# Kernel tuning notes

Measured on AMD Instinct MI355X. Metric: run time of the kernel, lower is better.

The kernel has to match this reference:

```python
import jax, jax.numpy as jnp
import numpy as np

B, T, E = 4, 2048, 1024
H, HS = 16, 64
FF = 4 * E
EPS = 1e-5


def _layer_norm(x, g, b):
    mu = jnp.mean(x, axis=-1, keepdims=True)
    var = jnp.mean(jnp.square(x - mu), axis=-1, keepdims=True)
    return (x - mu) * jax.lax.rsqrt(var + EPS) * g + b


def setup_inputs() -> dict:
    key = jax.random.key(0)
    ks = jax.random.split(key, 8)
    s_e = 1.0 / np.sqrt(E)
    s_hs = 1.0 / np.sqrt(H * HS)
    s_ff = 1.0 / np.sqrt(FF)
    return {
        "x": jax.random.normal(ks[0], (B, T, E), dtype=jnp.float32),
        # weights stored as [in, out] (transpose of torch's [out, in])
        "qkv_w": jax.random.uniform(ks[1], (E, 3 * H * HS), minval=-s_e, maxval=s_e),
        "attn_proj_w": jax.random.uniform(ks[2], (H * HS, E), minval=-s_hs, maxval=s_hs),
        "attn_proj_b": jax.random.uniform(ks[3], (E,), minval=-s_hs, maxval=s_hs),
        "ln1_g": jnp.ones((E,), jnp.float32),
        "ln1_b": jnp.zeros((E,), jnp.float32),
        "ln2_g": jnp.ones((E,), jnp.float32),
        "ln2_b": jnp.zeros((E,), jnp.float32),
        "ff_w1": jax.random.uniform(ks[4], (E, FF), minval=-s_e, maxval=s_e),
        "ff_b1": jax.random.uniform(ks[5], (FF,), minval=-s_e, maxval=s_e),
        "ff_w2": jax.random.uniform(ks[6], (FF, E), minval=-s_ff, maxval=s_ff),
        "ff_b2": jax.random.uniform(ks[7], (E,), minval=-s_ff, maxval=s_ff),
    }


def reference(x, qkv_w, attn_proj_w, attn_proj_b, ln1_g, ln1_b, ln2_g, ln2_b,
              ff_w1, ff_b1, ff_w2, ff_b2):
    b, t, _ = x.shape
    # --- pre-LN causal self-attention ---
    h = _layer_norm(x, ln1_g, ln1_b)
    qkv = h @ qkv_w                                  # [B,T,3*H*HS]
    q, k, v = jnp.split(qkv, 3, axis=-1)
    q = q.reshape(b, t, H, HS).transpose(0, 2, 1, 3)  # [B,H,T,HS]
    k = k.reshape(b, t, H, HS).transpose(0, 2, 1, 3)
    v = v.reshape(b, t, H, HS).transpose(0, 2, 1, 3)
    scores = jnp.einsum('bhqd,bhkd->bhqk', q, k) * (HS ** -0.5)
    causal = jnp.tril(jnp.ones((t, t), dtype=bool))
    scores = jnp.where(causal, scores, -jnp.inf)
    attn = jax.nn.softmax(scores, axis=-1)
    out = jnp.einsum('bhqk,bhkd->bhqd', attn, v)      # [B,H,T,HS]
    out = out.transpose(0, 2, 1, 3).reshape(b, t, H * HS)
    x = x + out @ attn_proj_w + attn_proj_b
    # --- pre-LN feed-forward ---
    h2 = _layer_norm(x, ln2_g, ln2_b)
    ff = jax.nn.relu(h2 @ ff_w1 + ff_b1) @ ff_w2 + ff_b2
    return x + ff
```

## Files before the change

### kernel.cpp

```cpp
#include <hip/hip_runtime.h>
#include <math.h>

#define B_ 4
#define T_ 2048
#define E_ 1024
#define H_ 16
#define HS_ 64
#define FF_ 4096
#define M_ (B_ * T_)
#define QKV3_ (3 * H_ * HS_)

typedef short bf16x8 __attribute__((ext_vector_type(8)));
typedef short bf16x4 __attribute__((ext_vector_type(4)));
typedef float f32x4 __attribute__((ext_vector_type(4)));

__device__ __forceinline__ unsigned short f2bf(float f) {
    unsigned int u = __float_as_uint(f);
    return (unsigned short)((u + 0x7fffu + ((u >> 16) & 1u)) >> 16);
}

__device__ __forceinline__ void gload16(const void* g, void* l) {
    __builtin_amdgcn_global_load_lds(
        (const __attribute__((address_space(1))) void*)g,
        (__attribute__((address_space(3))) void*)l, 16, 0, 0);
}

__global__ __launch_bounds__(256) void wT_bf16(const float* __restrict__ W,
                                               unsigned short* __restrict__ WT,
                                               int K, int N) {
    __shared__ float t[32][33];
    const int n0 = blockIdx.x * 32, k0 = blockIdx.y * 32;
    const int tid = threadIdx.x;
#pragma unroll
    for (int i = 0; i < 4; i++) {
        const int idx = i * 256 + tid;
        const int r = idx >> 5, c = idx & 31;
        t[r][c] = W[(size_t)(k0 + r) * N + n0 + c];
    }
    __syncthreads();
#pragma unroll
    for (int i = 0; i < 4; i++) {
        const int idx = i * 256 + tid;
        const int n = idx >> 5, k = idx & 31;
        WT[(size_t)(n0 + n) * K + k0 + k] = f2bf(t[k][n]);
    }
}

__global__ __launch_bounds__(256) void ln_bf16(const float* __restrict__ x,
                                               const float* __restrict__ g,
                                               const float* __restrict__ b,
                                               unsigned short* __restrict__ out) {
    const int row = blockIdx.x;
    const int tid = threadIdx.x;
    const float4 v = ((const float4*)(x + (size_t)row * E_))[tid];
    float s = v.x + v.y + v.z + v.w;
    float ss = v.x * v.x + v.y * v.y + v.z * v.z + v.w * v.w;
    for (int off = 32; off > 0; off >>= 1) {
        s += __shfl_down(s, off);
        ss += __shfl_down(ss, off);
    }
    __shared__ float rs[4], rss[4];
    const int wid = tid >> 6;
    if ((tid & 63) == 0) { rs[wid] = s; rss[wid] = ss; }
    __syncthreads();
    const float tot = rs[0] + rs[1] + rs[2] + rs[3];
    const float tot2 = rss[0] + rss[1] + rss[2] + rss[3];
    const float mean = tot * (1.0f / E_);
    const float var = tot2 * (1.0f / E_) - mean * mean;
    const float rstd = rsqrtf(var + 1e-5f);
    const float4 gv = ((const float4*)g)[tid];
    const float4 bv = ((const float4*)b)[tid];
    ushort4 o;
    o.x = f2bf((v.x - mean) * rstd * gv.x + bv.x);
    o.y = f2bf((v.y - mean) * rstd * gv.y + bv.y);
    o.z = f2bf((v.z - mean) * rstd * gv.z + bv.z);
    o.w = f2bf((v.w - mean) * rstd * gv.w + bv.w);
    ((ushort4*)(out + (size_t)row * E_))[tid] = o;
}

__device__ __forceinline__ void stage_half(const unsigned short* __restrict__ G,
                                           size_t rbase, int K, int k0,
                                           unsigned short* lds, int c) {
    const int r = c >> 3, s = c & 7;
    gload16(G + rbase + (size_t)r * K + k0 + ((s ^ (r & 7)) * 8),
            (char*)lds + c * 16);
}

template <bool BIASF, bool RELU, bool RES, bool OUTBF16>
__global__ __launch_bounds__(512) void gemm_v3(
    const unsigned short* __restrict__ A,
    const unsigned short* __restrict__ BT,
    const float* __restrict__ bias,
    const float* __restrict__ res,
    float* __restrict__ Cf,
    unsigned short* __restrict__ Cb,
    int M, int N, int K) {
    __shared__ unsigned short As[3][128 * 64];
    __shared__ unsigned short Bs[3][256 * 64];

    const int tid = threadIdx.x;
    const int lane = tid & 63;
    const int w = tid >> 6;
    const int wm = w >> 2, wn = w & 3;
    const int lm = lane & 15;
    const int kg = lane >> 4;

    const int gx = gridDim.x;
    const int nwg = gx * gridDim.y;
    const int lin = blockIdx.y * gx + blockIdx.x;
    const int cpx = nwg >> 3;
    const int swz = (lin & 7) * cpx + (lin >> 3);
    const int rowBase = (swz / gx) * 128, colBase = (swz % gx) * 256;

    const size_t rA = (size_t)rowBase * K;
    const size_t rB = (size_t)colBase * K;

    f32x4 acc[4][4];
#pragma unroll
    for (int mt = 0; mt < 4; mt++)
#pragma unroll
        for (int nt = 0; nt < 4; nt++)
#pragma unroll
            for (int r = 0; r < 4; r++) acc[mt][nt][r] = 0.0f;

    const int nk = K >> 6;
#pragma unroll
    for (int h = 0; h < 2; h++) {
        stage_half(A, rA, K, 0, As[0], h * 512 + tid);
        stage_half(BT, rB, K, 0, Bs[0], h * 1024 + tid);
        stage_half(BT, rB, K, 0, Bs[0], h * 1024 + 512 + tid);
    }
#pragma unroll
    for (int h = 0; h < 2; h++) {
        stage_half(A, rA, K, 64, As[1], h * 512 + tid);
        stage_half(BT, rB, K, 64, Bs[1], h * 1024 + tid);
        stage_half(BT, rB, K, 64, Bs[1], h * 1024 + 512 + tid);
    }
    asm volatile("s_waitcnt vmcnt(6)" ::: "memory");
    __builtin_amdgcn_s_barrier();
    __builtin_amdgcn_sched_barrier(0);

    for (int t = 0; t < nk; ++t) {
        const int cur = t % 3;
        const int nx2 = (t + 2) % 3;
        const bool doStage = (t + 2 < nk);
#pragma unroll
        for (int ks = 0; ks < 2; ++ks) {
            bf16x8 af[4], bfr[4];
#pragma unroll
            for (int mt = 0; mt < 4; mt++) {
                const int r = wm * 64 + mt * 16 + lm;
                af[mt] = *(const bf16x8*)(As[cur] + r * 64 +
                                          (((ks * 4 + kg) ^ (r & 7)) * 8));
            }
#pragma unroll
            for (int nt = 0; nt < 4; nt++) {
                const int r = wn * 64 + nt * 16 + lm;
                bfr[nt] = *(const bf16x8*)(Bs[cur] + r * 64 +
                                           (((ks * 4 + kg) ^ (r & 7)) * 8));
            }
            if (doStage) {
                stage_half(A, rA, K, (t + 2) * 64, As[nx2], ks * 512 + tid);
                stage_half(BT, rB, K, (t + 2) * 64, Bs[nx2], ks * 1024 + tid);
                stage_half(BT, rB, K, (t + 2) * 64, Bs[nx2], ks * 1024 + 512 + tid);
            }
            __builtin_amdgcn_s_barrier();
            __builtin_amdgcn_sched_barrier(0);
            __builtin_amdgcn_s_setprio(1);
#pragma unroll
            for (int mt = 0; mt < 4; mt++)
#pragma unroll
                for (int nt = 0; nt < 4; nt++)
                    acc[mt][nt] = __builtin_amdgcn_mfma_f32_16x16x32_bf16(
                        af[mt], bfr[nt], acc[mt][nt], 0, 0, 0);
            __builtin_amdgcn_s_setprio(0);
            if (ks == 0) {
                __builtin_amdgcn_s_barrier();
                __builtin_amdgcn_sched_barrier(0);
            }
        }
        if (t + 2 < nk) {
            asm volatile("s_waitcnt vmcnt(6)" ::: "memory");
        } else if (t + 1 < nk) {
            asm volatile("s_waitcnt vmcnt(0)" ::: "memory");
        }
        __builtin_amdgcn_sched_barrier(0);
        __builtin_amdgcn_s_barrier();
        __builtin_amdgcn_sched_barrier(0);
    }

#pragma unroll
    for (int mt = 0; mt < 4; mt++) {
#pragma unroll
        for (int nt = 0; nt < 4; nt++) {
            const int cg = colBase + wn * 64 + nt * 16 + lm;
#pragma unroll
            for (int r = 0; r < 4; r++) {
                const int rg = rowBase + wm * 64 + mt * 16 + kg * 4 + r;
                float v = acc[mt][nt][r];
                if (BIASF) v += bias[cg];
                if (RELU) v = fmaxf(v, 0.0f);
                if (RES) v += res[(size_t)rg * N + cg];
                if (OUTBF16) Cb[(size_t)rg * N + cg] = f2bf(v);
                else Cf[(size_t)rg * N + cg] = v;
            }
        }
    }
}

__global__ __launch_bounds__(256) void attn_mfma3(const unsigned short* __restrict__ qkv,
                                                  unsigned short* __restrict__ out) {
    __shared__ unsigned short Ks[2][64 * 64];
    __shared__ unsigned short Vt[2][64 * 72];

    const int tid = threadIdx.x;
    const int lane = tid & 63;
    const int w = tid >> 6;
    const int lm = lane & 15;
    const int kg = lane >> 4;
    const int qt = 15 - blockIdx.x;
    const int bh = blockIdx.y;
    const int b = bh >> 4, h = bh & 15;
    const int bT = b * T_;
    const int q0w = qt * 128 + w * 32;
    const float K1 = 0.18033688011f;

    bf16x8 qf[2][2];
#pragma unroll
    for (int qg = 0; qg < 2; qg++) {
        const size_t qo = (size_t)(bT + q0w + qg * 16 + lm) * QKV3_ + h * HS_;
#pragma unroll
        for (int dc = 0; dc < 2; dc++)
            qf[qg][dc] = *(const bf16x8*)(qkv + qo + dc * 32 + kg * 8);
    }

    f32x4 o[2][4];
#pragma unroll
    for (int qg = 0; qg < 2; qg++)
#pragma unroll
        for (int dt = 0; dt < 4; dt++)
#pragma unroll
            for (int r = 0; r < 4; r++) o[qg][dt][r] = 0.0f;
    float m2[2] = {-INFINITY, -INFINITY};
    float l[2] = {0.0f, 0.0f};

    const int rK = tid >> 3, chK = tid & 7;
    const int sK = (chK ^ (rK & 7)) * 8;
    const int rp = tid >> 3, chV = tid & 7;
    const int vws = (2 * rp) ^ (chV << 2);

    const size_t hK = E_ + h * HS_;
    const size_t hV = 2 * E_ + h * HS_;
    bf16x8 kA, kB, vA, vB;

#define LOADT(kvb)                                                                          \
    do {                                                                                    \
        kA = *(const bf16x8*)(qkv + (size_t)(bT + (kvb) + rK) * QKV3_ + hK + chK * 8);      \
        kB = *(const bf16x8*)(qkv + (size_t)(bT + (kvb) + rK + 32) * QKV3_ + hK + chK * 8); \
        vA = *(const bf16x8*)(qkv + (size_t)(bT + (kvb) + 2 * rp) * QKV3_ + hV + chV * 8);  \
        vB = *(const bf16x8*)(qkv + (size_t)(bT + (kvb) + 2 * rp + 1) * QKV3_ + hV + chV * 8); \
    } while (0)

    const int nt = 2 * (qt + 1);
    LOADT(0);
    for (int t = 0; t < nt; t++) {
        const int kvbase = t * 64;
        const int cb = t & 1;
        *(bf16x8*)(Ks[cb] + rK * 64 + sK) = kA;
        *(bf16x8*)(Ks[cb] + (rK + 32) * 64 + sK) = kB;
#pragma unroll
        for (int i = 0; i < 8; i++) {
            const unsigned int pv = (unsigned int)(unsigned short)vA[i] |
                                    ((unsigned int)(unsigned short)vB[i] << 16);
            *(unsigned int*)(Vt[cb] + (chV * 8 + i) * 72 + vws) = pv;
        }
        if (t + 1 < nt) LOADT((t + 1) * 64);
        asm volatile("s_waitcnt lgkmcnt(0)" ::: "memory");
        __builtin_amdgcn_s_barrier();
        __builtin_amdgcn_sched_barrier(0);
        if (kvbase > q0w + 31) continue;

        bf16x8 af[4][2];
#pragma unroll
        for (int g = 0; g < 4; g++)
#pragma unroll
            for (int dc = 0; dc < 2; dc++)
                af[g][dc] = *(const bf16x8*)(Ks[cb] + (g * 16 + lm) * 64 +
                                             (((dc * 4 + kg) ^ (lm & 7)) * 8));

        bf16x8 pa[2][2];
#pragma unroll
        for (int qg = 0; qg < 2; qg++) {
            f32x4 z = {0.0f, 0.0f, 0.0f, 0.0f};
            f32x4 s[4];
#pragma unroll
            for (int g = 0; g < 4; g++) {
                s[g] = __builtin_amdgcn_mfma_f32_16x16x32_bf16(af[g][0], qf[qg][0], z, 0, 0, 0);
                s[g] = __builtin_amdgcn_mfma_f32_16x16x32_bf16(af[g][1], qf[qg][1], s[g], 0, 0, 0);
            }
            const int qrow = q0w + qg * 16 + lm;
            float sv[16];
#pragma unroll
            for (int g = 0; g < 4; g++)
#pragma unroll
                for (int r = 0; r < 4; r++) sv[g * 4 + r] = s[g][r];
            if (kvbase + 63 > q0w + qg * 16) {
#pragma unroll
                for (int g = 0; g < 4; g++)
#pragma unroll
                    for (int r = 0; r < 4; r++) {
                        const int kv = kvbase + g * 16 + kg * 4 + r;
                        if (kv > qrow) sv[g * 4 + r] = -INFINITY;
                    }
            }
            const float mx = fmaxf(
                fmaxf(fmaxf(fmaxf(sv[0], sv[1]), fmaxf(sv[2], sv[3])),
                      fmaxf(fmaxf(sv[4], sv[5]), fmaxf(sv[6], sv[7]))),
                fmaxf(fmaxf(fmaxf(sv[8], sv[9]), fmaxf(sv[10], sv[11])),
                      fmaxf(fmaxf(sv[12], sv[13]), fmaxf(sv[14], sv[15]))));
            float mxw = fmaxf(mx, __shfl_xor(mx, 16));
            mxw = fmaxf(mxw, __shfl_xor(mxw, 32));
            const float mx2 = mxw * K1;
            if (!__all(m2[qg] > -1e30f && mx2 <= m2[qg] + 11.5f)) {
                const float m2new = fmaxf(m2[qg], mx2);
                const float alpha = exp2f(m2[qg] - m2new);
#pragma unroll
                for (int r = 0; r < 4; r++) {
                    const float ar = __shfl(alpha, kg * 4 + r);
#pragma unroll
                    for (int dt = 0; dt < 4; dt++) o[qg][dt][r] *= ar;
                }
                l[qg] *= alpha;
                m2[qg] = m2new;
            }
            float p[16];
#pragma unroll
            for (int j = 0; j < 16; j++) p[j] = exp2f(fmaf(sv[j], K1, -m2[qg]));
            float ls = (((p[0] + p[1]) + (p[2] + p[3])) + ((p[4] + p[5]) + (p[6] + p[7]))) +
                       (((p[8] + p[9]) + (p[10] + p[11])) + ((p[12] + p[13]) + (p[14] + p[15])));
            ls += __shfl_xor(ls, 16);
            ls += __shfl_xor(ls, 32);
            l[qg] += ls;
#pragma unroll
            for (int j = 0; j < 8; j++) {
                ((unsigned short*)&pa[qg][0])[j] = f2bf(p[j]);
                ((unsigned short*)&pa[qg][1])[j] = f2bf(p[8 + j]);
            }
        }

#pragma unroll
        for (int dt = 0; dt < 4; dt++) {
            const int drow = dt * 16 + lm;
            const unsigned short* vrow = Vt[cb] + drow * 72;
            const int xo = (kg * 4) ^ (((drow >> 3) & 7) << 2);
#pragma unroll
            for (int c = 0; c < 2; c++) {
                const bf16x4 lo = *(const bf16x4*)(vrow + c * 32 + xo);
                const bf16x4 hi = *(const bf16x4*)(vrow + c * 32 + (xo ^ 16));
                const bf16x8 vf = __builtin_shufflevector(lo, hi, 0, 1, 2, 3, 4, 5, 6, 7);
                o[0][dt] = __builtin_amdgcn_mfma_f32_16x16x32_bf16(pa[0][c], vf, o[0][dt], 0, 0, 0);
                o[1][dt] = __builtin_amdgcn_mfma_f32_16x16x32_bf16(pa[1][c], vf, o[1][dt], 0, 0, 0);
            }
        }
    }
#undef LOADT

#pragma unroll
    for (int qg = 0; qg < 2; qg++)
#pragma unroll
        for (int r = 0; r < 4; r++) {
            const float li = 1.0f / __shfl(l[qg], kg * 4 + r);
            const size_t ro = (size_t)(bT + q0w + qg * 16 + kg * 4 + r) * E_ + h * HS_;
#pragma unroll
            for (int dt = 0; dt < 4; dt++)
                out[ro + dt * 16 + lm] = f2bf(o[qg][dt][r] * li);
        }
}

extern "C" void kernel_launch(void* const* d_in, const int* in_sizes, int n_in,
                              void* d_out, int out_size, void* d_ws, size_t ws_size,
                              hipStream_t stream) {
    const float* x           = (const float*)d_in[0];
    const float* qkv_w       = (const float*)d_in[1];
    const float* attn_proj_w = (const float*)d_in[2];
    const float* attn_proj_b = (const float*)d_in[3];
    const float* ln1_g       = (const float*)d_in[4];
    const float* ln1_b       = (const float*)d_in[5];
    const float* ln2_g       = (const float*)d_in[6];
    const float* ln2_b       = (const float*)d_in[7];
    const float* ff_w1       = (const float*)d_in[8];
    const float* ff_b1       = (const float*)d_in[9];
    const float* ff_w2       = (const float*)d_in[10];
    const float* ff_b2       = (const float*)d_in[11];
    float* out = (float*)d_out;
    char* wsb = (char*)d_ws;

    unsigned short* wqkvT  = (unsigned short*)(wsb + 0);
    unsigned short* wprojT = (unsigned short*)(wsb + 6291456);
    unsigned short* wff1T  = (unsigned short*)(wsb + 8388608);
    unsigned short* wff2T  = (unsigned short*)(wsb + 16777216);
    unsigned short* hbuf   = (unsigned short*)(wsb + 25165824);
    unsigned short* attnb  = (unsigned short*)(wsb + 41943040);
    unsigned short* qkvb   = (unsigned short*)(wsb + 58720256);
    unsigned short* ff1b   = qkvb;

    wT_bf16<<<dim3(QKV3_ / 32, E_ / 32), 256, 0, stream>>>(qkv_w, wqkvT, E_, QKV3_);
    wT_bf16<<<dim3(E_ / 32, E_ / 32), 256, 0, stream>>>(attn_proj_w, wprojT, E_, E_);
    wT_bf16<<<dim3(FF_ / 32, E_ / 32), 256, 0, stream>>>(ff_w1, wff1T, E_, FF_);
    wT_bf16<<<dim3(E_ / 32, FF_ / 32), 256, 0, stream>>>(ff_w2, wff2T, FF_, E_);

    ln_bf16<<<M_, 256, 0, stream>>>(x, ln1_g, ln1_b, hbuf);
    gemm_v3<false, false, false, true><<<dim3(QKV3_ / 256, M_ / 128), 512, 0, stream>>>(
        hbuf, wqkvT, nullptr, nullptr, nullptr, qkvb, M_, QKV3_, E_);
    attn_mfma3<<<dim3(T_ / 128, B_ * H_), 256, 0, stream>>>(qkvb, attnb);
    gemm_v3<true, false, true, false><<<dim3(E_ / 256, M_ / 128), 512, 0, stream>>>(
        attnb, wprojT, attn_proj_b, x, out, nullptr, M_, E_, E_);
    ln_bf16<<<M_, 256, 0, stream>>>(out, ln2_g, ln2_b, hbuf);
    gemm_v3<true, true, false, true><<<dim3(FF_ / 256, M_ / 128), 512, 0, stream>>>(
        hbuf, wff1T, ff_b1, nullptr, nullptr, ff1b, M_, FF_, E_);
    gemm_v3<true, false, true, false><<<dim3(E_ / 256, M_ / 128), 512, 0, stream>>>(
        ff1b, wff2T, ff_b2, out, out, nullptr, M_, E_, FF_);
    (void)ws_size; (void)in_sizes; (void)n_in; (void)out_size;
}
```

Baseline: 570.7 us.

## Enlarge GEMM row tile to 256 with templated N tile and double buffering

Replaces the 128x256 triple-buffered GEMM with a templated kernel using 256-row tiles, a configurable N tile (256 for QKV/FF1, 128 for proj/FF2) and a two-stage LDS buffer. Loads for the next k-tile are issued at the start of each iteration and fully drained at the end. The aim is higher data reuse per block and fewer barriers per iteration. The risks are weaker latency hiding from shallower pipelining, larger register use from more accumulators, and fewer blocks for the N=1024 GEMMs.

```diff
diff --git a/kernel.cpp b/kernel.cpp
--- a/kernel.cpp
+++ b/kernel.cpp
@@ -86,8 +86,8 @@
             (char*)lds + c * 16);
 }
 
-template <bool BIASF, bool RELU, bool RES, bool OUTBF16>
-__global__ __launch_bounds__(512) void gemm_v3(
+template <int BN, int NWN, bool BIASF, bool RELU, bool RES, bool OUTBF16>
+__global__ __launch_bounds__(512, 2) void gemm_v4(
     const unsigned short* __restrict__ A,
     const unsigned short* __restrict__ BT,
     const float* __restrict__ bias,
@@ -95,13 +95,18 @@
     float* __restrict__ Cf,
     unsigned short* __restrict__ Cb,
     int M, int N, int K) {
-    __shared__ unsigned short As[3][128 * 64];
-    __shared__ unsigned short Bs[3][256 * 64];
+    constexpr int NWM = 8 / NWN;
+    constexpr int MW = 256 / NWM;
+    constexpr int M_REP = MW / 16;
+    constexpr int BPT = (BN * 64 / 8) / 512;
+
+    __shared__ unsigned short As[2][256 * 64];
+    __shared__ unsigned short Bs[2][BN * 64];
 
     const int tid = threadIdx.x;
     const int lane = tid & 63;
     const int w = tid >> 6;
-    const int wm = w >> 2, wn = w & 3;
+    const int wm = w / NWN, wn = w % NWN;
     const int lm = lane & 15;
     const int kg = lane >> 4;
 
@@ -110,14 +115,14 @@
     const int lin = blockIdx.y * gx + blockIdx.x;
     const int cpx = nwg >> 3;
     const int swz = (lin & 7) * cpx + (lin >> 3);
-    const int rowBase = (swz / gx) * 128, colBase = (swz % gx) * 256;
+    const int rowBase = (swz / gx) * 256, colBase = (swz % gx) * BN;
 
     const size_t rA = (size_t)rowBase * K;
     const size_t rB = (size_t)colBase * K;
 
-    f32x4 acc[4][4];
-#pragma unroll
-    for (int mt = 0; mt < 4; mt++)
+    f32x4 acc[M_REP][4];
+#pragma unroll
+    for (int mt = 0; mt < M_REP; mt++)
 #pragma unroll
         for (int nt = 0; nt < 4; nt++)
 #pragma unroll
@@ -125,31 +130,29 @@
 
     const int nk = K >> 6;
 #pragma unroll
-    for (int h = 0; h < 2; h++) {
-        stage_half(A, rA, K, 0, As[0], h * 512 + tid);
-        stage_half(BT, rB, K, 0, Bs[0], h * 1024 + tid);
-        stage_half(BT, rB, K, 0, Bs[0], h * 1024 + 512 + tid);
-    }
-#pragma unroll
-    for (int h = 0; h < 2; h++) {
-        stage_half(A, rA, K, 64, As[1], h * 512 + tid);
-        stage_half(BT, rB, K, 64, Bs[1], h * 1024 + tid);
-        stage_half(BT, rB, K, 64, Bs[1], h * 1024 + 512 + tid);
-    }
-    asm volatile("s_waitcnt vmcnt(6)" ::: "memory");
+    for (int i = 0; i < 4; i++) stage_half(A, rA, K, 0, As[0], i * 512 + tid);
+#pragma unroll
+    for (int i = 0; i < BPT; i++) stage_half(BT, rB, K, 0, Bs[0], i * 512 + tid);
+    asm volatile("s_waitcnt vmcnt(0)" ::: "memory");
     __builtin_amdgcn_s_barrier();
     __builtin_amdgcn_sched_barrier(0);
 
     for (int t = 0; t < nk; ++t) {
-        const int cur = t % 3;
-        const int nx2 = (t + 2) % 3;
-        const bool doStage = (t + 2 < nk);
+        const int cur = t & 1;
+        if (t + 1 < nk) {
+#pragma unroll
+            for (int i = 0; i < 4; i++)
+                stage_half(A, rA, K, (t + 1) * 64, As[cur ^ 1], i * 512 + tid);
+#pragma unroll
+            for (int i = 0; i < BPT; i++)
+                stage_half(BT, rB, K, (t + 1) * 64, Bs[cur ^ 1], i * 512 + tid);
+        }
 #pragma unroll
         for (int ks = 0; ks < 2; ++ks) {
-            bf16x8 af[4], bfr[4];
-#pragma unroll
-            for (int mt = 0; mt < 4; mt++) {
-                const int r = wm * 64 + mt * 16 + lm;
+            bf16x8 af[M_REP], bfr[4];
+#pragma unroll
+            for (int mt = 0; mt < M_REP; mt++) {
+                const int r = wm * MW + mt * 16 + lm;
                 af[mt] = *(const bf16x8*)(As[cur] + r * 64 +
                                           (((ks * 4 + kg) ^ (r & 7)) * 8));
             }
@@ -159,44 +162,30 @@
                 bfr[nt] = *(const bf16x8*)(Bs[cur] + r * 64 +
                                            (((ks * 4 + kg) ^ (r & 7)) * 8));
             }
-            if (doStage) {
-                stage_half(A, rA, K, (t + 2) * 64, As[nx2], ks * 512 + tid);
-                stage_half(BT, rB, K, (t + 2) * 64, Bs[nx2], ks * 1024 + tid);
-                stage_half(BT, rB, K, (t + 2) * 64, Bs[nx2], ks * 1024 + 512 + tid);
-            }
-            __builtin_amdgcn_s_barrier();
-            __builtin_amdgcn_sched_barrier(0);
             __builtin_amdgcn_s_setprio(1);
 #pragma unroll
-            for (int mt = 0; mt < 4; mt++)
+            for (int mt = 0; mt < M_REP; mt++)
 #pragma unroll
                 for (int nt = 0; nt < 4; nt++)
                     acc[mt][nt] = __builtin_amdgcn_mfma_f32_16x16x32_bf16(
                         af[mt], bfr[nt], acc[mt][nt], 0, 0, 0);
             __builtin_amdgcn_s_setprio(0);
-            if (ks == 0) {
-                __builtin_amdgcn_s_barrier();
-                __builtin_amdgcn_sched_barrier(0);
-            }
-        }
-        if (t + 2 < nk) {
-            asm volatile("s_waitcnt vmcnt(6)" ::: "memory");
-        } else if (t + 1 < nk) {
+        }
+        if (t + 1 < nk) {
             asm volatile("s_waitcnt vmcnt(0)" ::: "memory");
-        }
-        __builtin_amdgcn_sched_barrier(0);
-        __builtin_amdgcn_s_barrier();
-        __builtin_amdgcn_sched_barrier(0);
-    }
-
-#pragma unroll
-    for (int mt = 0; mt < 4; mt++) {
+            __builtin_amdgcn_s_barrier();
+            __builtin_amdgcn_sched_barrier(0);
+        }
+    }
+
+#pragma unroll
+    for (int mt = 0; mt < M_REP; mt++) {
 #pragma unroll
         for (int nt = 0; nt < 4; nt++) {
             const int cg = colBase + wn * 64 + nt * 16 + lm;
 #pragma unroll
             for (int r = 0; r < 4; r++) {
-                const int rg = rowBase + wm * 64 + mt * 16 + kg * 4 + r;
+                const int rg = rowBase + wm * MW + mt * 16 + kg * 4 + r;
                 float v = acc[mt][nt][r];
                 if (BIASF) v += bias[cg];
                 if (RELU) v = fmaxf(v, 0.0f);
@@ -410,15 +399,15 @@
     wT_bf16<<<dim3(E_ / 32, FF_ / 32), 256, 0, stream>>>(ff_w2, wff2T, FF_, E_);
 
     ln_bf16<<<M_, 256, 0, stream>>>(x, ln1_g, ln1_b, hbuf);
-    gemm_v3<false, false, false, true><<<dim3(QKV3_ / 256, M_ / 128), 512, 0, stream>>>(
+    gemm_v4<256, 4, false, false, false, true><<<dim3(QKV3_ / 256, M_ / 256), 512, 0, stream>>>(
         hbuf, wqkvT, nullptr, nullptr, nullptr, qkvb, M_, QKV3_, E_);
     attn_mfma3<<<dim3(T_ / 128, B_ * H_), 256, 0, stream>>>(qkvb, attnb);
-    gemm_v3<true, false, true, false><<<dim3(E_ / 256, M_ / 128), 512, 0, stream>>>(
+    gemm_v4<128, 2, true, false, true, false><<<dim3(E_ / 128, M_ / 256), 512, 0, stream>>>(
         attnb, wprojT, attn_proj_b, x, out, nullptr, M_, E_, E_);
     ln_bf16<<<M_, 256, 0, stream>>>(out, ln2_g, ln2_b, hbuf);
-    gemm_v3<true, true, false, true><<<dim3(FF_ / 256, M_ / 128), 512, 0, stream>>>(
+    gemm_v4<256, 4, true, true, false, true><<<dim3(FF_ / 256, M_ / 256), 512, 0, stream>>>(
         hbuf, wff1T, ff_b1, nullptr, nullptr, ff1b, M_, FF_, E_);
-    gemm_v3<true, false, true, false><<<dim3(E_ / 256, M_ / 128), 512, 0, stream>>>(
+    gemm_v4<128, 2, true, false, true, false><<<dim3(E_ / 128, M_ / 256), 512, 0, stream>>>(
         ff1b, wff2T, ff_b2, out, out, nullptr, M_, E_, FF_);
     (void)ws_size; (void)in_sizes; (void)n_in; (void)out_size;
 }
```

New measurement: 583.3 us. 1.02x slower.
